# Kernel tuning notes

Hardware: AMD Instinct MI355X
Metric: run time of the kernel (lower is better)

## Reference

```python
import jax, jax.numpy as jnp
import numpy as np

DROP_P = 0.5
DROP_KEY = jax.random.key(42)  # fixed key: deterministic dropout mask


def setup_inputs() -> dict:
    key = jax.random.key(0)
    k1, k2, k3 = jax.random.split(key, 3)
    B, H, S, D = 2, 16, 2048, 128
    x1 = jax.random.normal(k1, (B, H, S, D), dtype=jnp.float32)
    x2 = jax.random.normal(k2, (B, H, S, D), dtype=jnp.float32)
    # broadcastable per-head divisor; offset to keep it away from zero
    x3 = jax.random.uniform(k3, (B, H, 1, 1), dtype=jnp.float32) + 1.0
    return {"x1": x1, "x2": x2, "x3": x3}


def reference(x1, x2, x3):
    # v1 = x1 @ x2^T  -> [B,H,S,S]; v2 = v1 / x3 (broadcast divisor)
    scores = jnp.einsum('bhqd,bhkd->bhqk', x1, x2) / x3
    # v3 = softmax over last dim
    probs = jax.nn.softmax(scores, axis=-1)
    # v4 = dropout(p=0.5), training=True semantics: mask and rescale by 1/(1-p)
    keep = jax.random.bernoulli(DROP_KEY, 1.0 - DROP_P, probs.shape)
    probs = jnp.where(keep, probs / (1.0 - DROP_P), 0.0)
    # v5 = v4 @ x1 (note: values are x1, not a separate V); v6 = v5 + x2 residual
    out = jnp.einsum('bhqk,bhkd->bhqd', probs, x1) + x2
    return out
```

## Files before the change

kernel.cpp:

```cpp
#include <hip/hip_runtime.h>
#include <math.h>


constexpr int Sc = 2048, Dc = 128;
constexpr int NT = 32;
constexpr int VOFF = 16384;
constexpr int POFF = 32768;

typedef short bf16x8 __attribute__((ext_vector_type(8)));
typedef float f32x4 __attribute__((ext_vector_type(4)));
union U8 { uint4 u; bf16x8 v; };

__device__ __forceinline__ unsigned rotl(unsigned x, int r) {
  return __builtin_amdgcn_alignbit(x, x, 32 - r);
}

__device__ __forceinline__ void tf2x32(unsigned x0, unsigned x1,
                                       unsigned &o0, unsigned &o1) {
  const unsigned ks0 = 0u, ks1 = 42u;
  const unsigned ks2 = 0x1BD11BDAu ^ 0u ^ 42u;
  x0 += ks0; x1 += ks1;
#define TFR(r) { x0 += x1; x1 = rotl(x1, r); x1 ^= x0; }
  TFR(13) TFR(15) TFR(26) TFR(6)
  x0 += ks1; x1 += ks2 + 1u;
  TFR(17) TFR(29) TFR(16) TFR(24)
  x0 += ks2; x1 += ks0 + 2u;
  TFR(13) TFR(15) TFR(26) TFR(6)
  x0 += ks0; x1 += ks1 + 3u;
  TFR(17) TFR(29) TFR(16) TFR(24)
  x0 += ks1; x1 += ks2 + 4u;
  TFR(13) TFR(15) TFR(26) TFR(6)
  x0 += ks2; x1 += ks0 + 5u;
#undef TFR
  o0 = x0; o1 = x1;
}

__device__ __forceinline__ unsigned keepmask(unsigned idx) {
  unsigned a, b; tf2x32(0u, idx, a, b);
  (void)b;
  return (unsigned)(((int)~a) >> 31);
}

__device__ __forceinline__ unsigned pk2rn(float a, float b) {
  return __builtin_amdgcn_perm(__float_as_uint(b) + 0x8000u,
                               __float_as_uint(a) + 0x8000u, 0x07060302u);
}

__device__ __forceinline__ unsigned hw2(unsigned ma, unsigned mb) {
  return __builtin_amdgcn_perm(mb, ma, 0x05040100u);
}

__device__ __forceinline__ void gload16(const void* g, void* l) {
  __builtin_amdgcn_global_load_lds(
      (const __attribute__((address_space(1))) void*)g,
      (__attribute__((address_space(3))) void*)l, 16, 0, 0);
}

__global__ __launch_bounds__(256)
void prepack(const float* __restrict__ x1, const float* __restrict__ x2,
             uint4* __restrict__ Kb, uint4* __restrict__ Vt) {
  __shared__ ushort Kl[32 * 136];
  __shared__ ushort Vl[32 * 136];
  const int tid = threadIdx.x;
  const size_t tile = blockIdx.x;
  const float4* ks = (const float4*)(x2 + tile * 4096);
  const float4* vs = (const float4*)(x1 + tile * 4096);
#pragma unroll
  for (int it = 0; it < 4; ++it) {
    int f = it * 256 + tid;
    int row = f >> 5, c4 = f & 31;
    float4 kv = ks[f];
    float4 vv = vs[f];
    *(uint2*)&Kl[row * 136 + c4 * 4] = uint2{pk2rn(kv.x, kv.y), pk2rn(kv.z, kv.w)};
    *(uint2*)&Vl[row * 136 + c4 * 4] = uint2{pk2rn(vv.x, vv.y), pk2rn(vv.z, vv.w)};
  }
  __syncthreads();
#pragma unroll
  for (int it = 0; it < 2; ++it) {
    int u = it * 256 + tid;
    int lane = u & 63, grp = u >> 6;
    int mt = grp >> 2, c = grp & 3, m16 = lane & 15, g = lane >> 4;
    Kb[tile * 512 + u] = *(const uint4*)&Kl[(mt * 16 + m16) * 136 + c * 32 + g * 8];
  }
#pragma unroll
  for (int it = 0; it < 2; ++it) {
    int u = it * 256 + tid;
    int lane = u & 63, dt = u >> 6, m16 = lane & 15, g = lane >> 4;
    int d = dt * 16 + m16, k0 = g * 8;
    unsigned w[4];
#pragma unroll
    for (int p = 0; p < 4; ++p) {
      unsigned lo = Vl[(k0 + 2 * p) * 136 + d];
      unsigned hi = Vl[(k0 + 2 * p + 1) * 136 + d];
      w[p] = lo | (hi << 16);
    }
    Vt[tile * 512 + u] = uint4{w[0], w[1], w[2], w[3]};
  }
}

__global__ __launch_bounds__(256, 4)
void attn6(const uint4* __restrict__ Kb, const uint4* __restrict__ Vt,
           const float* __restrict__ x1, const float* __restrict__ x2,
           const float* __restrict__ x3, float* __restrict__ out) {
  __shared__ uint4 smemv[40960 / 16];
  char* smem = (char*)smemv;
  float* Os = (float*)smem;

  const int tid = threadIdx.x, wave = tid >> 6, lane = tid & 63;
  const int g = lane >> 4, q = lane & 15;
  const int blk = blockIdx.x, bh = blk & 31, qt = blk >> 5;

  const float* X1 = x1 + (size_t)bh * (Sc * Dc);
  const float* X2 = x2 + (size_t)bh * (Sc * Dc);
  float* outp = out + (size_t)bh * (Sc * Dc);
  const float cl2 = (1.0f / x3[bh]) * 1.4426950408889634f;

  const int qrow = qt * 64 + wave * 16 + q;
  const unsigned row_base = (unsigned)(bh * Sc + qrow) * (unsigned)Sc;
  char* prow = smem + POFF + wave * 2048 + q * 128;

  bf16x8 qf[4];
  {
    const float4* qsrc = (const float4*)(X1 + (size_t)qrow * Dc);
#pragma unroll
    for (int c = 0; c < 4; ++c) {
      float4 f0 = qsrc[c * 8 + g * 2], f1 = qsrc[c * 8 + g * 2 + 1];
      U8 cv; cv.u = uint4{pk2rn(f0.x, f0.y), pk2rn(f0.z, f0.w),
                          pk2rn(f1.x, f1.y), pk2rn(f1.z, f1.w)};
      qf[c] = cv.v;
    }
  }

  f32x4 o[8];
#pragma unroll
  for (int i = 0; i < 8; ++i) o[i] = f32x4{0.f, 0.f, 0.f, 0.f};
  float l_run = 0.0f;
  const size_t tg = (size_t)bh * 64;

  for (int t = 0; t < NT; ++t) {
    __syncthreads();
    {
      const char* kg = (const char*)(Kb + (tg + 2 * t) * 512);
      const char* vg = (const char*)(Vt + (tg + 2 * t) * 512);
      const int off = wave * 1024 + lane * 16;
#pragma unroll
      for (int h = 0; h < 2; ++h) {
        gload16(kg + h * 8192 + off,        smem + h * 8192 + off);
        gload16(kg + h * 8192 + off + 4096, smem + h * 8192 + off + 4096);
        gload16(vg + h * 8192 + off,        smem + VOFF + h * 8192 + off);
        gload16(vg + h * 8192 + off + 4096, smem + VOFF + h * 8192 + off + 4096);
      }
    }
    __builtin_amdgcn_sched_barrier(0);

    unsigned km[8];
    {
      const unsigned ib = row_base + (unsigned)(t * 64) + (unsigned)(g * 4);
#pragma unroll
      for (int h2 = 0; h2 < 4; ++h2) {
        unsigned a0 = keepmask(ib + h2 * 16 + 0), a1 = keepmask(ib + h2 * 16 + 1);
        unsigned a2 = keepmask(ib + h2 * 16 + 2), a3 = keepmask(ib + h2 * 16 + 3);
        km[h2 * 2 + 0] = hw2(a0, a1);
        km[h2 * 2 + 1] = hw2(a2, a3);
      }
    }
    __syncthreads();

    f32x4 s0 = {}, s1 = {}, s2 = {}, s3 = {};
#pragma unroll
    for (int c = 0; c < 4; ++c) {
      U8 a0; a0.u = *(const uint4*)(smem +        ((0 * 4 + c) * 64 + lane) * 16);
      U8 a1; a1.u = *(const uint4*)(smem +        ((1 * 4 + c) * 64 + lane) * 16);
      U8 a2; a2.u = *(const uint4*)(smem + 8192 + ((0 * 4 + c) * 64 + lane) * 16);
      U8 a3; a3.u = *(const uint4*)(smem + 8192 + ((1 * 4 + c) * 64 + lane) * 16);
      s0 = __builtin_amdgcn_mfma_f32_16x16x32_bf16(a0.v, qf[c], s0, 0, 0, 0);
      s1 = __builtin_amdgcn_mfma_f32_16x16x32_bf16(a1.v, qf[c], s1, 0, 0, 0);
      s2 = __builtin_amdgcn_mfma_f32_16x16x32_bf16(a2.v, qf[c], s2, 0, 0, 0);
      s3 = __builtin_amdgcn_mfma_f32_16x16x32_bf16(a3.v, qf[c], s3, 0, 0, 0);
    }

    float pr[16];
    float ls = 0.0f;
#pragma unroll
    for (int i = 0; i < 4; ++i) { pr[i]      = __builtin_amdgcn_exp2f(s0[i] * cl2); ls += pr[i]; }
#pragma unroll
    for (int i = 0; i < 4; ++i) { pr[4 + i]  = __builtin_amdgcn_exp2f(s1[i] * cl2); ls += pr[4 + i]; }
#pragma unroll
    for (int i = 0; i < 4; ++i) { pr[8 + i]  = __builtin_amdgcn_exp2f(s2[i] * cl2); ls += pr[8 + i]; }
#pragma unroll
    for (int i = 0; i < 4; ++i) { pr[12 + i] = __builtin_amdgcn_exp2f(s3[i] * cl2); ls += pr[12 + i]; }
    ls += __shfl_xor(ls, 16);
    ls += __shfl_xor(ls, 32);
    l_run += ls;

#pragma unroll
    for (int h2 = 0; h2 < 4; ++h2) {
      unsigned w0 = pk2rn(pr[h2 * 4 + 0], pr[h2 * 4 + 1]) & km[h2 * 2 + 0];
      unsigned w1 = pk2rn(pr[h2 * 4 + 2], pr[h2 * 4 + 3]) & km[h2 * 2 + 1];
      int u = (h2 >> 1) * 8 + (h2 & 1) * 4 + g;
      *(uint2*)(prow + ((u ^ q) & 15) * 8) = uint2{w0, w1};
    }

    U8 bf0, bf1;
    {
      int u0 = 2 * g;
      uint2 lo0 = *(const uint2*)(prow + (((u0 + 0) ^ q) & 15) * 8);
      uint2 hi0 = *(const uint2*)(prow + (((u0 + 1) ^ q) & 15) * 8);
      bf0.u = uint4{lo0.x, lo0.y, hi0.x, hi0.y};
      int u1 = 8 + 2 * g;
      uint2 lo1 = *(const uint2*)(prow + (((u1 + 0) ^ q) & 15) * 8);
      uint2 hi1 = *(const uint2*)(prow + (((u1 + 1) ^ q) & 15) * 8);
      bf1.u = uint4{lo1.x, lo1.y, hi1.x, hi1.y};
    }

#pragma unroll
    for (int dt = 0; dt < 8; ++dt) {
      U8 av0; av0.u = *(const uint4*)(smem + VOFF +        (dt * 64 + lane) * 16);
      U8 av1; av1.u = *(const uint4*)(smem + VOFF + 8192 + (dt * 64 + lane) * 16);
      o[dt] = __builtin_amdgcn_mfma_f32_16x16x32_bf16(av0.v, bf0.v, o[dt], 0, 0, 0);
      o[dt] = __builtin_amdgcn_mfma_f32_16x16x32_bf16(av1.v, bf1.v, o[dt], 0, 0, 0);
    }
  }

  const float invl = 2.0f / l_run;
  __syncthreads();
  {
    float* ow = Os + (size_t)(wave * 16 + q) * 132;
#pragma unroll
    for (int dt = 0; dt < 8; ++dt) {
      int d = dt * 16 + g * 4;
      *(float4*)&ow[d] = float4{o[dt][0] * invl, o[dt][1] * invl,
                                o[dt][2] * invl, o[dt][3] * invl};
    }
  }
  __syncthreads();
#pragma unroll
  for (int it = 0; it < 8; ++it) {
    int f = it * 256 + tid;
    int ql = f >> 5, c4 = f & 31;
    float4 ov = *(const float4*)&Os[ql * 132 + c4 * 4];
    size_t goff = (size_t)(qt * 64 + ql) * Dc + c4 * 4;
    float4 xv = *(const float4*)&X2[goff];
    *(float4*)&outp[goff] = float4{ov.x + xv.x, ov.y + xv.y, ov.z + xv.z, ov.w + xv.w};
  }
}

extern "C" void kernel_launch(void* const* d_in, const int* in_sizes, int n_in,
                              void* d_out, int out_size, void* d_ws, size_t ws_size,
                              hipStream_t stream) {
  const float* x1 = (const float*)d_in[0];
  const float* x2 = (const float*)d_in[1];
  const float* x3 = (const float*)d_in[2];
  float* out = (float*)d_out;
  const size_t PREP = (size_t)2048 * 512 * 16;
  uint4* Kb = (uint4*)d_ws;
  uint4* Vtg = (uint4*)((char*)d_ws + PREP);
  prepack<<<2048, 256, 0, stream>>>(x1, x2, Kb, Vtg);
  attn6<<<1024, 256, 0, stream>>>(Kb, Vtg, x1, x2, x3, out);
}
```

Before: 398.1 us.

## Double-buffer K/V tiles in LDS and precompute next dropout masks

The attention kernel now double-buffers the K and V tiles in LDS. It issues the global-to-LDS loads for tile t+1 before computing tile t, which removes the second barrier per iteration. The dropout keep-masks for the next tile are generated after the QK MFMAs so the hash arithmetic can overlap with matrix work. The Threefry hash is trimmed to compute only the first output word, dropping the operations that only fed the unused second word. In exchange, LDS use per block roughly doubles and launch bounds drop to 2 blocks per CU, which lowers occupancy and may leave all 1024 blocks unable to be resident at once.

```diff
diff --git a/kernel.cpp b/kernel.cpp
--- a/kernel.cpp
+++ b/kernel.cpp
@@ -4,8 +4,9 @@
 
 constexpr int Sc = 2048, Dc = 128;
 constexpr int NT = 32;
-constexpr int VOFF = 16384;
-constexpr int POFF = 32768;
+constexpr int BUF = 32768;
+constexpr int VREL = 16384;
+constexpr int POFF = 65536;
 
 typedef short bf16x8 __attribute__((ext_vector_type(8)));
 typedef float f32x4 __attribute__((ext_vector_type(4)));
@@ -15,30 +16,28 @@
   return __builtin_amdgcn_alignbit(x, x, 32 - r);
 }
 
-__device__ __forceinline__ void tf2x32(unsigned x0, unsigned x1,
-                                       unsigned &o0, unsigned &o1) {
-  const unsigned ks0 = 0u, ks1 = 42u;
-  const unsigned ks2 = 0x1BD11BDAu ^ 0u ^ 42u;
-  x0 += ks0; x1 += ks1;
+__device__ __forceinline__ unsigned tf_o0(unsigned x1) {
+  const unsigned ks1 = 42u;
+  const unsigned ks2 = 0x1BD11BDAu ^ 42u;
+  unsigned x0 = 0u; x1 += ks1;
 #define TFR(r) { x0 += x1; x1 = rotl(x1, r); x1 ^= x0; }
   TFR(13) TFR(15) TFR(26) TFR(6)
   x0 += ks1; x1 += ks2 + 1u;
   TFR(17) TFR(29) TFR(16) TFR(24)
-  x0 += ks2; x1 += ks0 + 2u;
+  x0 += ks2; x1 += 0u + 2u;
   TFR(13) TFR(15) TFR(26) TFR(6)
-  x0 += ks0; x1 += ks1 + 3u;
+  x1 += ks1 + 3u;
   TFR(17) TFR(29) TFR(16) TFR(24)
   x0 += ks1; x1 += ks2 + 4u;
-  TFR(13) TFR(15) TFR(26) TFR(6)
-  x0 += ks2; x1 += ks0 + 5u;
+  TFR(13) TFR(15) TFR(26)
+  x0 += x1;
+  x0 += ks2;
 #undef TFR
-  o0 = x0; o1 = x1;
+  return x0;
 }
 
 __device__ __forceinline__ unsigned keepmask(unsigned idx) {
-  unsigned a, b; tf2x32(0u, idx, a, b);
-  (void)b;
-  return (unsigned)(((int)~a) >> 31);
+  return (unsigned)(((int)~tf_o0(idx)) >> 31);
 }
 
 __device__ __forceinline__ unsigned pk2rn(float a, float b) {
@@ -54,6 +53,16 @@
   __builtin_amdgcn_global_load_lds(
       (const __attribute__((address_space(1))) void*)g,
       (__attribute__((address_space(3))) void*)l, 16, 0, 0);
+}
+
+__device__ __forceinline__ void masks8(unsigned ib, unsigned km[8]) {
+#pragma unroll
+  for (int h2 = 0; h2 < 4; ++h2) {
+    unsigned a0 = keepmask(ib + h2 * 16 + 0), a1 = keepmask(ib + h2 * 16 + 1);
+    unsigned a2 = keepmask(ib + h2 * 16 + 2), a3 = keepmask(ib + h2 * 16 + 3);
+    km[h2 * 2 + 0] = hw2(a0, a1);
+    km[h2 * 2 + 1] = hw2(a2, a3);
+  }
 }
 
 __global__ __launch_bounds__(256)
@@ -98,11 +107,11 @@
   }
 }
 
-__global__ __launch_bounds__(256, 4)
-void attn6(const uint4* __restrict__ Kb, const uint4* __restrict__ Vt,
+__global__ __launch_bounds__(256, 2)
+void attn7(const uint4* __restrict__ Kb, const uint4* __restrict__ Vt,
            const float* __restrict__ x1, const float* __restrict__ x2,
            const float* __restrict__ x3, float* __restrict__ out) {
-  __shared__ uint4 smemv[40960 / 16];
+  __shared__ uint4 smemv[(POFF + 8192) / 16];
   char* smem = (char*)smemv;
   float* Os = (float*)smem;
 
@@ -118,6 +127,21 @@
   const int qrow = qt * 64 + wave * 16 + q;
   const unsigned row_base = (unsigned)(bh * Sc + qrow) * (unsigned)Sc;
   char* prow = smem + POFF + wave * 2048 + q * 128;
+
+  const size_t tg = (size_t)bh * 64;
+  const int off = wave * 1024 + lane * 16;
+
+  auto issue = [&](int tt, int bb) {
+    const char* kg = (const char*)(Kb + (tg + 2 * tt) * 512);
+    const char* vg = (const char*)(Vt + (tg + 2 * tt) * 512);
+#pragma unroll
+    for (int h = 0; h < 2; ++h) {
+      gload16(kg + h * 8192 + off,        smem + bb + h * 8192 + off);
+      gload16(kg + h * 8192 + off + 4096, smem + bb + h * 8192 + off + 4096);
+      gload16(vg + h * 8192 + off,        smem + bb + VREL + h * 8192 + off);
+      gload16(vg + h * 8192 + off + 4096, smem + bb + VREL + h * 8192 + off + 4096);
+    }
+  };
 
   bf16x8 qf[4];
   {
@@ -135,50 +159,37 @@
 #pragma unroll
   for (int i = 0; i < 8; ++i) o[i] = f32x4{0.f, 0.f, 0.f, 0.f};
   float l_run = 0.0f;
-  const size_t tg = (size_t)bh * 64;
+
+  issue(0, 0);
+  __builtin_amdgcn_sched_barrier(0);
+  unsigned kmc[8], kmn[8];
+  masks8(row_base + (unsigned)(g * 4), kmc);
 
   for (int t = 0; t < NT; ++t) {
     __syncthreads();
-    {
-      const char* kg = (const char*)(Kb + (tg + 2 * t) * 512);
-      const char* vg = (const char*)(Vt + (tg + 2 * t) * 512);
-      const int off = wave * 1024 + lane * 16;
-#pragma unroll
-      for (int h = 0; h < 2; ++h) {
-        gload16(kg + h * 8192 + off,        smem + h * 8192 + off);
-        gload16(kg + h * 8192 + off + 4096, smem + h * 8192 + off + 4096);
-        gload16(vg + h * 8192 + off,        smem + VOFF + h * 8192 + off);
-        gload16(vg + h * 8192 + off + 4096, smem + VOFF + h * 8192 + off + 4096);
-      }
-    }
+
+    if (t < NT - 1) issue(t + 1, ((t + 1) & 1) * BUF);
     __builtin_amdgcn_sched_barrier(0);
 
-    unsigned km[8];
-    {
-      const unsigned ib = row_base + (unsigned)(t * 64) + (unsigned)(g * 4);
-#pragma unroll
-      for (int h2 = 0; h2 < 4; ++h2) {
-        unsigned a0 = keepmask(ib + h2 * 16 + 0), a1 = keepmask(ib + h2 * 16 + 1);
-        unsigned a2 = keepmask(ib + h2 * 16 + 2), a3 = keepmask(ib + h2 * 16 + 3);
-        km[h2 * 2 + 0] = hw2(a0, a1);
-        km[h2 * 2 + 1] = hw2(a2, a3);
-      }
-    }
-    __syncthreads();
+    const char* kb = smem + (t & 1) * BUF;
+    const char* vb = kb + VREL;
 
     f32x4 s0 = {}, s1 = {}, s2 = {}, s3 = {};
 #pragma unroll
     for (int c = 0; c < 4; ++c) {
-      U8 a0; a0.u = *(const uint4*)(smem +        ((0 * 4 + c) * 64 + lane) * 16);
-      U8 a1; a1.u = *(const uint4*)(smem +        ((1 * 4 + c) * 64 + lane) * 16);
-      U8 a2; a2.u = *(const uint4*)(smem + 8192 + ((0 * 4 + c) * 64 + lane) * 16);
-      U8 a3; a3.u = *(const uint4*)(smem + 8192 + ((1 * 4 + c) * 64 + lane) * 16);
+      U8 a0; a0.u = *(const uint4*)(kb +        ((0 * 4 + c) * 64 + lane) * 16);
+      U8 a1; a1.u = *(const uint4*)(kb +        ((1 * 4 + c) * 64 + lane) * 16);
+      U8 a2; a2.u = *(const uint4*)(kb + 8192 + ((0 * 4 + c) * 64 + lane) * 16);
+      U8 a3; a3.u = *(const uint4*)(kb + 8192 + ((1 * 4 + c) * 64 + lane) * 16);
       s0 = __builtin_amdgcn_mfma_f32_16x16x32_bf16(a0.v, qf[c], s0, 0, 0, 0);
       s1 = __builtin_amdgcn_mfma_f32_16x16x32_bf16(a1.v, qf[c], s1, 0, 0, 0);
       s2 = __builtin_amdgcn_mfma_f32_16x16x32_bf16(a2.v, qf[c], s2, 0, 0, 0);
       s3 = __builtin_amdgcn_mfma_f32_16x16x32_bf16(a3.v, qf[c], s3, 0, 0, 0);
     }
 
+    if (t < NT - 1)
+      masks8(row_base + (unsigned)((t + 1) * 64) + (unsigned)(g * 4), kmn);
+
     float pr[16];
     float ls = 0.0f;
 #pragma unroll
@@ -195,8 +206,8 @@
 
 #pragma unroll
     for (int h2 = 0; h2 < 4; ++h2) {
-      unsigned w0 = pk2rn(pr[h2 * 4 + 0], pr[h2 * 4 + 1]) & km[h2 * 2 + 0];
-      unsigned w1 = pk2rn(pr[h2 * 4 + 2], pr[h2 * 4 + 3]) & km[h2 * 2 + 1];
+      unsigned w0 = pk2rn(pr[h2 * 4 + 0], pr[h2 * 4 + 1]) & kmc[h2 * 2 + 0];
+      unsigned w1 = pk2rn(pr[h2 * 4 + 2], pr[h2 * 4 + 3]) & kmc[h2 * 2 + 1];
       int u = (h2 >> 1) * 8 + (h2 & 1) * 4 + g;
       *(uint2*)(prow + ((u ^ q) & 15) * 8) = uint2{w0, w1};
     }
@@ -215,11 +226,14 @@
 
 #pragma unroll
     for (int dt = 0; dt < 8; ++dt) {
-      U8 av0; av0.u = *(const uint4*)(smem + VOFF +        (dt * 64 + lane) * 16);
-      U8 av1; av1.u = *(const uint4*)(smem + VOFF + 8192 + (dt * 64 + lane) * 16);
+      U8 av0; av0.u = *(const uint4*)(vb +        (dt * 64 + lane) * 16);
+      U8 av1; av1.u = *(const uint4*)(vb + 8192 + (dt * 64 + lane) * 16);
       o[dt] = __builtin_amdgcn_mfma_f32_16x16x32_bf16(av0.v, bf0.v, o[dt], 0, 0, 0);
       o[dt] = __builtin_amdgcn_mfma_f32_16x16x32_bf16(av1.v, bf1.v, o[dt], 0, 0, 0);
     }
+
+#pragma unroll
+    for (int i = 0; i < 8; ++i) kmc[i] = kmn[i];
   }
 
   const float invl = 2.0f / l_run;
@@ -256,5 +270,5 @@
   uint4* Kb = (uint4*)d_ws;
   uint4* Vtg = (uint4*)((char*)d_ws + PREP);
   prepack<<<2048, 256, 0, stream>>>(x1, x2, Kb, Vtg);
-  attn6<<<1024, 256, 0, stream>>>(Kb, Vtg, x1, x2, x3, out);
-}
+  attn7<<<1024, 256, 0, stream>>>(Kb, Vtg, x1, x2, x3, out);
+}
```

New measurement: 402.5 us. About the same (+1.1%).
